# Performance work log

Hardware: AMD Instinct MI355X
Metric: run time of the kernel (lower is better)

The kernel has to match this reference:

```python
import jax, jax.numpy as jnp
import numpy as np

B, S, T = 32, 512, 128   # batch, source chars, target (protoform) chars
V, L = 128, 5            # char vocab len(C2I), number of languages
E, H, F = 512, 1024, 2048  # embedding_dim, model_size, feedforward_dim
START_CHAR, SEP_LANG = 1, L - 1


def setup_inputs() -> dict:
    key = jax.random.key(0)
    ks = jax.random.split(key, 32)
    f32 = jnp.float32

    def n(k, shape, fan_in):
        return jax.random.normal(k, shape, dtype=f32) * (1.0 / np.sqrt(fan_in))

    inp = {
        "src_chars": jax.random.randint(ks[0], (B, S), 0, V),
        "src_langs": jax.random.randint(ks[1], (B, S), 0, L),
        "tgt_chars": jax.random.randint(ks[2], (B, T), 0, V),
        # embedding feature extractor
        "char_emb": jax.random.normal(ks[3], (V, E), dtype=f32) * 0.02,
        "lang_emb": jax.random.normal(ks[4], (L, E), dtype=f32) * 0.02,
        "fc_W": n(ks[5], (E, 2 * E), 2 * E),
        "fc_b": jnp.zeros((E,), f32),
        # encoder GRU (PyTorch gate layout r,z,n)
        "enc_Wi": n(ks[6], (3 * H, E), E),
        "enc_Wh": n(ks[7], (3 * H, H), H),
        "enc_bi": jnp.zeros((3 * H,), f32),
        "enc_bh": jnp.zeros((3 * H,), f32),
        # decoder GRU, input = [E ; H]
        "dec_Wi": n(ks[8], (3 * H, E + H), E + H),
        "dec_Wh": n(ks[9], (3 * H, H), H),
        "dec_bi": jnp.zeros((3 * H,), f32),
        "dec_bh": jnp.zeros((3 * H,), f32),
        # attention
        "Wq": n(ks[10], (H, H), H),
        "Wk": n(ks[11], (H, H), H),
        "Wcs": n(ks[12], (H, E), E),
        # MLP H -> 2F -> F -> V
        "W1": n(ks[13], (2 * F, H), H),
        "b1": jnp.zeros((2 * F,), f32),
        "W2": n(ks[14], (F, 2 * F), 2 * F),
        "b2": jnp.zeros((F,), f32),
        "W3": n(ks[15], (V, F), F),
    }
    return inp


def _gru_step(h, x, Wi, Wh, bi, bh):
    gi = x @ Wi.T + bi            # [B, 3H]
    gh = h @ Wh.T + bh            # [B, 3H]
    ir, iz, inn = jnp.split(gi, 3, axis=-1)
    hr, hz, hn = jnp.split(gh, 3, axis=-1)
    r = jax.nn.sigmoid(ir + hr)
    z = jax.nn.sigmoid(iz + hz)
    n = jnp.tanh(inn + r * hn)
    return (1.0 - z) * n + z * h


def _mlp(x, W1, b1, W2, b2, W3):
    h = jax.nn.relu(x @ W1.T + b1)
    h = jax.nn.relu(h @ W2.T + b2)
    return h @ W3.T               # [B, V]


def reference(src_chars, src_langs, tgt_chars,
              char_emb, lang_emb, fc_W, fc_b,
              enc_Wi, enc_Wh, enc_bi, enc_bh,
              dec_Wi, dec_Wh, dec_bi, dec_bh,
              Wq, Wk, Wcs,
              W1, b1, W2, b2, W3):
    # --- feature extraction: concat(char_emb, lang_emb) -> Linear(2E -> E) ---
    def embed(c_idx, l_idx):
        ce = char_emb[c_idx]                       # [..., E]
        le = lang_emb[l_idx]                       # [..., E]
        return jnp.concatenate([ce, le], -1) @ fc_W.T + fc_b

    encoded = embed(src_chars, src_langs)          # [B, S, E]

    # --- encoder GRU over source chars ---
    def enc_step(h, x_t):
        h = _gru_step(h, x_t, enc_Wi, enc_Wh, enc_bi, enc_bh)
        return h, h

    h0 = jnp.zeros((encoded.shape[0], enc_Wh.shape[1]), encoded.dtype)
    _, enc_states = jax.lax.scan(enc_step, h0, jnp.swapaxes(encoded, 0, 1))
    enc_states = jnp.swapaxes(enc_states, 0, 1)    # [B, S, H]

    # precompute attention values: W_c_s(encoded) + W_key(keys)  [B, S, H]
    att_vals = encoded @ Wcs.T + enc_states @ Wk.T

    # --- initial decoder step: <s> embedding + last encoder state ---
    start_emb = embed(jnp.full((encoded.shape[0],), START_CHAR),
                      jnp.full((encoded.shape[0],), SEP_LANG))  # [B, E]
    context0 = enc_states[:, -1]                   # [B, H]
    d0 = jnp.zeros_like(context0)
    dec_h = _gru_step(d0, jnp.concatenate([start_emb, context0], -1),
                      dec_Wi, dec_Wh, dec_bi, dec_bh)

    tgt_emb = embed(tgt_chars, jnp.full_like(tgt_chars, SEP_LANG))  # [B, T, E]

    # --- decode T steps with teacher forcing ---
    def dec_step(carry, x_t):
        h, ctx = carry
        scores_t = _mlp(h + ctx, W1, b1, W2, b2, W3)           # [B, V]
        q = h @ Wq.T                                           # [B, H]
        att = jnp.einsum('bsh,bh->bs', enc_states, q)
        w = jax.nn.softmax(att, axis=-1)
        ctx_new = jnp.einsum('bs,bsh->bh', w, att_vals)        # [B, H]
        h_new = _gru_step(h, jnp.concatenate([x_t, ctx_new], -1),
                          dec_Wi, dec_Wh, dec_bi, dec_bh)
        return (h_new, ctx_new), scores_t

    (_, _), scores = jax.lax.scan(dec_step, (dec_h, context0),
                                  jnp.swapaxes(tgt_emb, 0, 1))
    return jnp.swapaxes(scores, 0, 1)              # [B, T, V]
```

## Files before the change

kernel.cpp:

```cpp
#include <hip/hip_runtime.h>
#include <math.h>


#define Bb 32
#define Ss 512
#define Tt 128
#define Vv 128
#define Hh 1024
#define H3 3072
#define APAD 40
#define NBE 64

typedef __attribute__((ext_vector_type(8))) short bf16x8;
typedef __attribute__((ext_vector_type(4))) float f32x4;

__device__ inline f32x4 mfma_bf16(bf16x8 a, bf16x8 b, f32x4 c) {
  return __builtin_amdgcn_mfma_f32_16x16x32_bf16(a, b, c, 0, 0, 0);
}
__device__ inline unsigned short f2bf(float f) {
  unsigned u = __builtin_bit_cast(unsigned, f);
  unsigned r = (u + 0x7fffu + ((u >> 16) & 1u)) >> 16;
  return (unsigned short)r;
}
__device__ inline float lof(unsigned u) { return __builtin_bit_cast(float, u << 16); }
__device__ inline float hif(unsigned u) { return __builtin_bit_cast(float, u & 0xffff0000u); }
__device__ inline float bf2f(unsigned short h) {
  return __builtin_bit_cast(float, ((unsigned)h) << 16);
}

#define O_ESBF   0UL
#define O_ESQ    33554432UL
#define O_AVBF   67108864UL
#define O_HCBF   100663296UL
#define O_WHE    109051904UL
#define O_WHD    115343360UL
#define O_WIC    121634816UL
#define O_WKB    127926272UL
#define O_WQT    130023424UL
#define O_W1B    132120576UL
#define O_W2B    140509184UL
#define O_W3B    157286400UL
#define O_XCAT   157810688UL
#define O_EMBFC  160432128UL
#define O_GITAB  161742848UL
#define O_AVTAB  169607168UL
#define O_DGIXT  172228608UL
#define O_GH     173801472UL
#define O_GI     174194688UL
#define O_H      174587904UL
#define O_HBF    174718976UL
#define O_CTX    174784512UL
#define O_CTXBF  174915584UL
#define O_ATTL   174981120UL

__global__ void k_xcat(const float* __restrict__ ce, const float* __restrict__ le,
                       float* __restrict__ xcat) {
  int row = blockIdx.x;
  int l = row >> 7, c = row & 127;
  int i = threadIdx.x * 4;
  float4 v;
  if (i < 512) v = *(const float4*)(ce + c * 512 + i);
  else         v = *(const float4*)(le + l * 512 + (i - 512));
  *(float4*)(xcat + (size_t)row * 1024 + i) = v;
}

__global__ void k_cltab(const int* __restrict__ sc, const int* __restrict__ sl,
                        int* __restrict__ cl, int* __restrict__ bar) {
  if (blockIdx.x == 0 && threadIdx.x == 0) *bar = 0;
  int i = blockIdx.x * 256 + threadIdx.x;
  int b = i >> 9, s = i & 511;
  cl[s * 32 + b] = sl[b * Ss + s] * 128 + sc[b * Ss + s];
}

__global__ void k_cvt(const float* __restrict__ src, int ld, int lc,
                      unsigned short* __restrict__ dst) {
  size_t i = ((size_t)blockIdx.x * 256 + threadIdx.x) * 8;
  size_t r = i >> lc;
  int c = (int)(i & ((1u << lc) - 1));
  const float* s = src + r * (size_t)ld + c;
  float4 v0 = *(const float4*)s;
  float4 v1 = *(const float4*)(s + 4);
  union { unsigned short us[8]; uint4 u; } o;
  o.us[0] = f2bf(v0.x); o.us[1] = f2bf(v0.y); o.us[2] = f2bf(v0.z); o.us[3] = f2bf(v0.w);
  o.us[4] = f2bf(v1.x); o.us[5] = f2bf(v1.y); o.us[6] = f2bf(v1.z); o.us[7] = f2bf(v1.w);
  *(uint4*)(dst + i) = o.u;
}

__global__ void k_transcvt(const float* __restrict__ in, unsigned short* __restrict__ out) {
  __shared__ float t[32][33];
  int c0 = blockIdx.x * 32, r0 = blockIdx.y * 32;
  int tx = threadIdx.x, ty = threadIdx.y;
  for (int i = ty; i < 32; i += 8)
    t[i][tx] = in[(size_t)(r0 + i) * 1024 + c0 + tx];
  __syncthreads();
  for (int i = ty; i < 32; i += 8)
    out[(size_t)(c0 + i) * 1024 + r0 + tx] = f2bf(t[tx][i]);
}

template <bool BIAS>
__global__ __launch_bounds__(256) void k_gemm(
    const float* __restrict__ A, int lda, const float* __restrict__ W, int ldw,
    const float* __restrict__ bias, float* __restrict__ C, int ldc, int K) {
  __shared__ float As[8][128];
  __shared__ float Ws[8][128];
  int tid = threadIdx.x;
  int n0 = blockIdx.x * 128, m0 = blockIdx.y * 128;
  int tx = tid & 15, ty = tid >> 4;
  int lrow = tid >> 1, lseg = (tid & 1) * 4;
  const float* Ap = A + (size_t)(m0 + lrow) * lda + lseg;
  const float* Wp = W + (size_t)(n0 + lrow) * ldw + lseg;
  float acc[8][8];
#pragma unroll
  for (int i = 0; i < 8; ++i)
#pragma unroll
    for (int j = 0; j < 8; ++j) acc[i][j] = 0.f;
  for (int kt = 0; kt < K; kt += 8) {
    float4 av = *(const float4*)(Ap + kt);
    float4 wv = *(const float4*)(Wp + kt);
    __syncthreads();
    As[lseg + 0][lrow] = av.x; As[lseg + 1][lrow] = av.y;
    As[lseg + 2][lrow] = av.z; As[lseg + 3][lrow] = av.w;
    Ws[lseg + 0][lrow] = wv.x; Ws[lseg + 1][lrow] = wv.y;
    Ws[lseg + 2][lrow] = wv.z; Ws[lseg + 3][lrow] = wv.w;
    __syncthreads();
#pragma unroll
    for (int kk = 0; kk < 8; ++kk) {
      float a[8], b[8];
      *(float4*)(a + 0) = *(const float4*)(&As[kk][ty * 8 + 0]);
      *(float4*)(a + 4) = *(const float4*)(&As[kk][ty * 8 + 4]);
      *(float4*)(b + 0) = *(const float4*)(&Ws[kk][tx * 8 + 0]);
      *(float4*)(b + 4) = *(const float4*)(&Ws[kk][tx * 8 + 4]);
#pragma unroll
      for (int i = 0; i < 8; ++i)
#pragma unroll
        for (int j = 0; j < 8; ++j) acc[i][j] = fmaf(a[i], b[j], acc[i][j]);
    }
  }
#pragma unroll
  for (int i = 0; i < 8; ++i) {
    int r = m0 + ty * 8 + i;
#pragma unroll
    for (int j = 0; j < 8; ++j) {
      int c = n0 + tx * 8 + j;
      float v = acc[i][j];
      if (BIAS) v += bias[c];
      C[(size_t)r * ldc + c] = v;
    }
  }
}

template <int EPI, bool RELU, bool BIAS>
__global__ __launch_bounds__(256) void k_bgemm(
    const unsigned short* __restrict__ A, int lda,
    const unsigned short* __restrict__ W, int ldw,
    const float* __restrict__ bias, void* __restrict__ Cout, int ldc, int K,
    const float* __restrict__ avtab, const int* __restrict__ gl,
    const int* __restrict__ gc) {
  __shared__ unsigned short As[128 * APAD];
  __shared__ unsigned short Bs[128 * APAD];
  int tid = threadIdx.x;
  int n0 = blockIdx.x * 128, m0 = blockIdx.y * 128;
  int w = tid >> 6, l = tid & 63;
  int mw = (w & 1) * 64, nw = (w >> 1) * 64;
  int lrow = tid >> 1, lk = (tid & 1) * 16;
  const unsigned short* Ap = A + (size_t)(m0 + lrow) * lda + lk;
  const unsigned short* Wp = W + (size_t)(n0 + lrow) * ldw + lk;
  int fr = l & 15, fk = (l >> 4) * 8;
  f32x4 acc[4][4];
#pragma unroll
  for (int i = 0; i < 4; ++i)
#pragma unroll
    for (int j = 0; j < 4; ++j) acc[i][j] = (f32x4){0.f, 0.f, 0.f, 0.f};
  for (int kt = 0; kt < K; kt += 32) {
    uint4 a0 = *(const uint4*)(Ap + kt);
    uint4 a1 = *(const uint4*)(Ap + kt + 8);
    uint4 b0 = *(const uint4*)(Wp + kt);
    uint4 b1 = *(const uint4*)(Wp + kt + 8);
    __syncthreads();
    *(uint4*)&As[lrow * APAD + lk] = a0;
    *(uint4*)&As[lrow * APAD + lk + 8] = a1;
    *(uint4*)&Bs[lrow * APAD + lk] = b0;
    *(uint4*)&Bs[lrow * APAD + lk + 8] = b1;
    __syncthreads();
    bf16x8 af[4], bfg[4];
#pragma unroll
    for (int i = 0; i < 4; ++i) af[i] = *(const bf16x8*)&As[(mw + i * 16 + fr) * APAD + fk];
#pragma unroll
    for (int j = 0; j < 4; ++j) bfg[j] = *(const bf16x8*)&Bs[(nw + j * 16 + fr) * APAD + fk];
#pragma unroll
    for (int i = 0; i < 4; ++i)
#pragma unroll
      for (int j = 0; j < 4; ++j) acc[i][j] = mfma_bf16(af[i], bfg[j], acc[i][j]);
  }
#pragma unroll
  for (int i = 0; i < 4; ++i)
#pragma unroll
    for (int j = 0; j < 4; ++j) {
      int col = n0 + nw + j * 16 + fr;
#pragma unroll
      for (int r = 0; r < 4; ++r) {
        int row = m0 + mw + i * 16 + (l >> 4) * 4 + r;
        float v = acc[i][j][r];
        if (BIAS) v += bias[col];
        if (RELU) v = fmaxf(v, 0.f);
        if (EPI == 0) {
          ((unsigned short*)Cout)[(size_t)row * ldc + col] = f2bf(v);
        } else if (EPI == 1) {
          int cl = gl[row] * 128 + gc[row];
          ((unsigned short*)Cout)[(size_t)row * ldc + col] =
              f2bf(v + avtab[(size_t)cl * 1024 + col]);
        } else {
          int tt = row >> 5, bb = row & 31;
          ((float*)Cout)[(size_t)bb * (Tt * Vv) + tt * Vv + col] = v;
        }
      }
    }
}

__global__ __launch_bounds__(512) void k_enc_pers(
    const unsigned short* __restrict__ Whe, const float* __restrict__ gitab,
    const int* __restrict__ cltab, const float* __restrict__ bh,
    float* __restrict__ h, unsigned short* __restrict__ hbf0,
    unsigned short* __restrict__ hbf1, unsigned short* __restrict__ esb,
    int* __restrict__ bar) {
  __shared__ unsigned short Ws[48 * 1024];
  __shared__ f32x4 red[8 * 6 * 64];
  int tid = threadIdx.x;
  int blk = blockIdx.x;
  int w = tid >> 6, l = tid & 63;
  int fr = l & 15, q = l >> 4;
  int j = blk * 16 + fr;
  {
    uint4* dst = (uint4*)Ws;
    const uint4* src = (const uint4*)Whe;
#pragma unroll
    for (int it = 0; it < 12; ++it) {
      int idx = it * 512 + tid;
      int lr = idx >> 7, c = idx & 127;
      int grow = (lr >> 4) * 1024 + blk * 16 + (lr & 15);
      dst[lr * 128 + (c ^ (lr & 7))] = src[(size_t)grow * 128 + c];
    }
  }
  float bhr = bh[j], bhz = bh[1024 + j], bhn = bh[2048 + j];
  float hold[4] = {0.f, 0.f, 0.f, 0.f};
  __syncthreads();
  const bf16x8* Wsv = (const bf16x8*)Ws;
  for (int s = 0; s < Ss; ++s) {
    unsigned short* wb = (s & 1) ? hbf1 : hbf0;
    const unsigned short* rb = (s & 1) ? hbf0 : hbf1;
    float gi0[4], gi1[4], gi2[4];
    if (w < 2) {
#pragma unroll
      for (int r = 0; r < 4; ++r) {
        int b = w * 16 + q * 4 + r;
        int c = cltab[s * 32 + b];
        const float* gp = gitab + (size_t)c * H3 + j;
        gi0[r] = gp[0]; gi1[r] = gp[1024]; gi2[r] = gp[2048];
      }
    }
    f32x4 acc[2][3];
#pragma unroll
    for (int m = 0; m < 2; ++m)
#pragma unroll
      for (int g = 0; g < 3; ++g) acc[m][g] = (f32x4){0.f, 0.f, 0.f, 0.f};
    if (s > 0) {
      int kb = w * 128 + q * 8;
      const unsigned short* A0 = rb + fr * 1024 + kb;
#pragma unroll
      for (int kt = 0; kt < 128; kt += 32) {
        bf16x8 a0 = *(const bf16x8*)(A0 + kt);
        bf16x8 a1 = *(const bf16x8*)(A0 + 16 * 1024 + kt);
        int c8 = (kb + kt) >> 3;
#pragma unroll
        for (int g = 0; g < 3; ++g) {
          bf16x8 bw = Wsv[(g * 16 + fr) * 128 + (c8 ^ (fr & 7))];
          acc[0][g] = mfma_bf16(a0, bw, acc[0][g]);
          acc[1][g] = mfma_bf16(a1, bw, acc[1][g]);
        }
      }
    }
#pragma unroll
    for (int m = 0; m < 2; ++m)
#pragma unroll
      for (int g = 0; g < 3; ++g)
        red[(w * 6 + m * 3 + g) * 64 + l] = acc[m][g];
    __syncthreads();
    if (w < 2) {
      int m = w;
      f32x4 as_[3];
#pragma unroll
      for (int g = 0; g < 3; ++g) as_[g] = (f32x4){0.f, 0.f, 0.f, 0.f};
#pragma unroll
      for (int ww = 0; ww < 8; ++ww)
#pragma unroll
        for (int g = 0; g < 3; ++g)
          as_[g] = as_[g] + red[(ww * 6 + m * 3 + g) * 64 + l];
#pragma unroll
      for (int r = 0; r < 4; ++r) {
        int b = m * 16 + q * 4 + r;
        float ghr = bhr, ghz = bhz, ghn = bhn;
        ghr += as_[0][r]; ghz += as_[1][r]; ghn += as_[2][r];
        float rg = 1.f / (1.f + expf(-(gi0[r] + ghr)));
        float zg = 1.f / (1.f + expf(-(gi1[r] + ghz)));
        float ng = tanhf(gi2[r] + rg * ghn);
        float hn = (1.f - zg) * ng + zg * hold[r];
        hold[r] = hn;
        unsigned short hb = f2bf(hn);
        wb[b * 1024 + j] = hb;
        esb[((size_t)b * Ss + s) * 1024 + j] = hb;
        if (s == Ss - 1) h[b * 1024 + j] = hn;
      }
    }
    __syncthreads();
    if (tid == 0) {
      __hip_atomic_fetch_add(bar, 1, __ATOMIC_RELEASE, __HIP_MEMORY_SCOPE_AGENT);
      int tgt = NBE * (s + 1);
      while (__hip_atomic_load(bar, __ATOMIC_RELAXED, __HIP_MEMORY_SCOPE_AGENT) < tgt)
        __builtin_amdgcn_s_sleep(1);
      __builtin_amdgcn_fence(__ATOMIC_ACQUIRE, "agent");
    }
    __syncthreads();
  }
}

template <int MODE>
__global__ __launch_bounds__(512) void k_step(
    const unsigned short* __restrict__ Wh,
    const unsigned short* __restrict__ Abf,
    const float* __restrict__ gtab,
    const int* __restrict__ idx,
    const float* __restrict__ ghb,
    const float* __restrict__ bh,
    float* __restrict__ h,
    unsigned short* __restrict__ hbfW,
    unsigned short* __restrict__ esb,
    int s, int flags) {
  __shared__ f32x4 red[8 * 6 * 64];
  int tid = threadIdx.x;
  int w = tid >> 6, l = tid & 63;
  int fr = l & 15, q = l >> 4;
  int j = blockIdx.x * 16 + fr;
  f32x4 acc[2][3];
#pragma unroll
  for (int m = 0; m < 2; ++m)
#pragma unroll
    for (int g = 0; g < 3; ++g) acc[m][g] = (f32x4){0.f, 0.f, 0.f, 0.f};
  if (!(flags & 4)) {
    int kb = w * 128 + q * 8;
    const unsigned short* A0 = Abf + fr * 1024 + kb;
    const unsigned short* W0 = Wh + (size_t)j * 1024 + kb;
#pragma unroll
    for (int kt = 0; kt < 128; kt += 32) {
      bf16x8 a0 = *(const bf16x8*)(A0 + kt);
      bf16x8 a1 = *(const bf16x8*)(A0 + 16 * 1024 + kt);
      bf16x8 b0 = *(const bf16x8*)(W0 + kt);
      bf16x8 b1 = *(const bf16x8*)(W0 + 1024 * 1024 + kt);
      bf16x8 b2 = *(const bf16x8*)(W0 + 2048 * 1024 + kt);
      acc[0][0] = mfma_bf16(a0, b0, acc[0][0]);
      acc[1][0] = mfma_bf16(a1, b0, acc[1][0]);
      acc[0][1] = mfma_bf16(a0, b1, acc[0][1]);
      acc[1][1] = mfma_bf16(a1, b1, acc[1][1]);
      acc[0][2] = mfma_bf16(a0, b2, acc[0][2]);
      acc[1][2] = mfma_bf16(a1, b2, acc[1][2]);
    }
  }
#pragma unroll
  for (int m = 0; m < 2; ++m)
#pragma unroll
    for (int g = 0; g < 3; ++g)
      red[(w * 6 + m * 3 + g) * 64 + l] = acc[m][g];
  __syncthreads();
  if (w >= 2) return;
  int m = w;
  f32x4 as_[3];
#pragma unroll
  for (int g = 0; g < 3; ++g) as_[g] = (f32x4){0.f, 0.f, 0.f, 0.f};
#pragma unroll
  for (int ww = 0; ww < 8; ++ww)
#pragma unroll
    for (int g = 0; g < 3; ++g)
      as_[g] = as_[g] + red[(ww * 6 + m * 3 + g) * 64 + l];
  float bhr = bh[j], bhz = bh[1024 + j], bhn = bh[2048 + j];
#pragma unroll
  for (int r = 0; r < 4; ++r) {
    int b = m * 16 + q * 4 + r;
    int c = (MODE == 0) ? idx[s * 32 + b] : ((flags & 2) ? 1 : idx[b * Tt + s]);
    const float* gp = gtab + (size_t)c * H3 + j;
    float gir = gp[0], giz = gp[1024], gin = gp[2048];
    float ghr = bhr, ghz = bhz, ghn = bhn;
    if (MODE == 0) {
      ghr += as_[0][r]; ghz += as_[1][r]; ghn += as_[2][r];
    } else {
      gir += as_[0][r]; giz += as_[1][r]; gin += as_[2][r];
      if (!(flags & 1)) {
        const float* g2 = ghb + b * H3 + j;
        ghr += g2[0]; ghz += g2[1024]; ghn += g2[2048];
      }
    }
    float rg = 1.f / (1.f + expf(-(gir + ghr)));
    float zg = 1.f / (1.f + expf(-(giz + ghz)));
    float ng = tanhf(gin + rg * ghn);
    float hold = (flags & 1) ? 0.f : h[b * 1024 + j];
    float hn = (1.f - zg) * ng + zg * hold;
    h[b * 1024 + j] = hn;
    unsigned short hb = f2bf(hn);
    hbfW[b * 1024 + j] = hb;
    if (MODE == 0) esb[((size_t)b * Ss + s) * 1024 + j] = hb;
  }
}

__global__ __launch_bounds__(256) void k_rec(
    const unsigned short* __restrict__ A, const unsigned short* __restrict__ W,
    float* __restrict__ C, int N, int nrec,
    const unsigned short* __restrict__ esq, const float* __restrict__ h,
    const float* __restrict__ ctx, float* __restrict__ attL,
    unsigned short* __restrict__ hc) {
  __shared__ unsigned short As[32 * 1024];
  int tid = threadIdx.x;
  int id = blockIdx.x;
  if (id < nrec) {
    {
      const uint4* src = (const uint4*)A;
      uint4* dst = (uint4*)As;
#pragma unroll
      for (int i = 0; i < 16; ++i) {
        int c = i * 256 + tid;
        int m = c >> 7, kc = c & 127;
        dst[m * 128 + (kc ^ (m & 7))] = src[c];
      }
    }
    __syncthreads();
    int w = tid >> 6, l = tid & 63;
    int nb = id * 64 + w * 16;
    int fr = l & 15, fk8 = (l >> 4);
    const unsigned short* Wp = W + (size_t)(nb + fr) * 1024 + fk8 * 8;
    const bf16x8* Asv = (const bf16x8*)As;
    f32x4 acc0 = (f32x4){0.f, 0.f, 0.f, 0.f}, acc1 = acc0;
#pragma unroll 8
    for (int kt = 0; kt < 1024; kt += 32) {
      int kc8 = (kt >> 3) + fk8;
      bf16x8 bw = *(const bf16x8*)(Wp + kt);
      bf16x8 a0 = Asv[fr * 128 + (kc8 ^ (fr & 7))];
      bf16x8 a1 = Asv[(fr + 16) * 128 + (kc8 ^ (fr & 7))];
      acc0 = mfma_bf16(a0, bw, acc0);
      acc1 = mfma_bf16(a1, bw, acc1);
    }
    int col = nb + fr;
    int rb = (l >> 4) * 4;
#pragma unroll
    for (int r = 0; r < 4; ++r) {
      C[(size_t)(rb + r) * N + col] = acc0[r];
      C[(size_t)(rb + r + 16) * N + col] = acc1[r];
    }
  } else {
    float* hs = (float*)As;
    int a = id - nrec, b = a >> 3, sc = a & 7;
    for (int i = tid; i < 1024; i += 256) hs[i] = h[b * 1024 + i];
    __syncthreads();
    if (sc < 4) {
      int j = sc * 256 + tid;
      hc[b * 1024 + j] = f2bf(hs[j] + ctx[b * 1024 + j]);
    }
    int sg = tid >> 2, li = tid & 3;
    int s = sc * 64 + sg;
    const unsigned short* ep = esq + (size_t)(b * 512 + s) * 1024;
    float acc = 0.f;
#pragma unroll 4
    for (int i = 0; i < 32; ++i) {
      int k = (i * 4 + li) * 8;
      uint4 e = *(const uint4*)(ep + k);
      float4 h0 = *(const float4*)&hs[k];
      float4 h1 = *(const float4*)&hs[k + 4];
      acc += lof(e.x) * h0.x + hif(e.x) * h0.y + lof(e.y) * h0.z + hif(e.y) * h0.w +
             lof(e.z) * h1.x + hif(e.z) * h1.y + lof(e.w) * h1.z + hif(e.w) * h1.w;
    }
    acc += __shfl_xor(acc, 1);
    acc += __shfl_xor(acc, 2);
    if (li == 0) attL[b * 512 + s] = acc;
  }
}

__global__ void k_ctxinit(const float* __restrict__ h, float* __restrict__ ctx,
                          unsigned short* __restrict__ ctxbf) {
  int idx = blockIdx.x * 256 + threadIdx.x;
  float v = h[idx];
  ctx[idx] = v;
  ctxbf[idx] = f2bf(v);
}

__global__ __launch_bounds__(256) void k_ctxsm(const float* __restrict__ attL,
                                               const unsigned short* __restrict__ av,
                                               float* __restrict__ ctx,
                                               unsigned short* __restrict__ ctxbf) {
  int jt = blockIdx.x, b = blockIdx.y;
  __shared__ float w[512];
  __shared__ float wm[4];
  __shared__ float wsm[4];
  __shared__ float red2[128];
  int tid = threadIdx.x;
  float a0 = attL[b * Ss + tid * 2];
  float a1 = attL[b * Ss + tid * 2 + 1];
  float m = fmaxf(a0, a1);
  for (int d = 1; d < 64; d <<= 1) m = fmaxf(m, __shfl_xor(m, d));
  if ((tid & 63) == 0) wm[tid >> 6] = m;
  __syncthreads();
  m = fmaxf(fmaxf(wm[0], wm[1]), fmaxf(wm[2], wm[3]));
  float e0 = expf(a0 - m), e1 = expf(a1 - m);
  w[tid * 2] = e0;
  w[tid * 2 + 1] = e1;
  float ssum = e0 + e1;
  for (int d = 1; d < 64; d <<= 1) ssum += __shfl_xor(ssum, d);
  if ((tid & 63) == 0) wsm[tid >> 6] = ssum;
  __syncthreads();
  float scale = 1.f / (wsm[0] + wsm[1] + wsm[2] + wsm[3]);
  int j = jt * 128 + (tid & 127);
  int sh = tid >> 7;
  const unsigned short* avp = av + (size_t)(b * Ss + sh * 256) * Hh + j;
  float acc = 0.f;
#pragma unroll 16
  for (int s = 0; s < 256; ++s) acc += w[sh * 256 + s] * bf2f(avp[(size_t)s * Hh]);
  if (sh == 1) red2[tid & 127] = acc;
  __syncthreads();
  if (sh == 0) {
    float v = (acc + red2[tid & 127]) * scale;
    ctx[b * Hh + j] = v;
    ctxbf[b * Hh + j] = f2bf(v);
  }
}

extern "C" void kernel_launch(void* const* d_in, const int* in_sizes, int n_in,
                              void* d_out, int out_size, void* d_ws, size_t ws_size,
                              hipStream_t stream) {
  (void)in_sizes; (void)n_in; (void)out_size; (void)ws_size;
  const int*   src_chars = (const int*)d_in[0];
  const int*   src_langs = (const int*)d_in[1];
  const int*   tgt_chars = (const int*)d_in[2];
  const float* char_emb  = (const float*)d_in[3];
  const float* lang_emb  = (const float*)d_in[4];
  const float* fc_W  = (const float*)d_in[5];
  const float* fc_b  = (const float*)d_in[6];
  const float* enc_Wi = (const float*)d_in[7];
  const float* enc_Wh = (const float*)d_in[8];
  const float* enc_bi = (const float*)d_in[9];
  const float* enc_bh = (const float*)d_in[10];
  const float* dec_Wi = (const float*)d_in[11];
  const float* dec_Wh = (const float*)d_in[12];
  const float* dec_bi = (const float*)d_in[13];
  const float* dec_bh = (const float*)d_in[14];
  const float* Wq  = (const float*)d_in[15];
  const float* Wk  = (const float*)d_in[16];
  const float* Wcs = (const float*)d_in[17];
  const float* W1 = (const float*)d_in[18];
  const float* b1 = (const float*)d_in[19];
  const float* W2 = (const float*)d_in[20];
  const float* b2 = (const float*)d_in[21];
  const float* W3 = (const float*)d_in[22];
  float* out = (float*)d_out;

  char* ws = (char*)d_ws;
  unsigned short* esbf  = (unsigned short*)(ws + O_ESBF);
  unsigned short* esq   = (unsigned short*)(ws + O_ESQ);
  unsigned short* avbf  = (unsigned short*)(ws + O_AVBF);
  unsigned short* hcbf  = (unsigned short*)(ws + O_HCBF);
  unsigned short* WheB  = (unsigned short*)(ws + O_WHE);
  unsigned short* WhdB  = (unsigned short*)(ws + O_WHD);
  unsigned short* WicB  = (unsigned short*)(ws + O_WIC);
  unsigned short* WkB   = (unsigned short*)(ws + O_WKB);
  unsigned short* WqTB  = (unsigned short*)(ws + O_WQT);
  unsigned short* W1B   = (unsigned short*)(ws + O_W1B);
  unsigned short* W2B   = (unsigned short*)(ws + O_W2B);
  unsigned short* W3B   = (unsigned short*)(ws + O_W3B);
  float* xcat   = (float*)(ws + O_XCAT);
  float* embfc  = (float*)(ws + O_EMBFC);
  float* gitab  = (float*)(ws + O_GITAB);
  float* avtab  = (float*)(ws + O_AVTAB);
  float* dgixt  = (float*)(ws + O_DGIXT);
  float* ghbuf  = (float*)(ws + O_GH);
  float* h      = (float*)(ws + O_H);
  unsigned short* hbf   = (unsigned short*)(ws + O_HBF);
  float* ctx    = (float*)(ws + O_CTX);
  unsigned short* ctxbf = (unsigned short*)(ws + O_CTXBF);
  float* attL   = (float*)(ws + O_ATTL);
  unsigned short* G1 = esq;
  unsigned short* G2 = avbf;
  int* cltab = (int*)(ws + O_GI);
  unsigned short* hbf2 = (unsigned short*)(ws + O_GI + 65536);
  int* bar = (int*)(ws + O_GI + 131072);

  dim3 blk(256);

  k_xcat<<<640, blk, 0, stream>>>(char_emb, lang_emb, xcat);
  k_cltab<<<64, blk, 0, stream>>>(src_chars, src_langs, cltab, bar);
  k_gemm<true><<<dim3(4, 5), blk, 0, stream>>>(xcat, 1024, fc_W, 1024, fc_b, embfc, 512, 1024);
  k_gemm<true><<<dim3(24, 5), blk, 0, stream>>>(embfc, 512, enc_Wi, 512, enc_bi, gitab, H3, 512);
  k_gemm<false><<<dim3(8, 5), blk, 0, stream>>>(embfc, 512, Wcs, 512, nullptr, avtab, Hh, 512);
  k_gemm<true><<<dim3(24, 1), blk, 0, stream>>>(embfc + 512 * 512, 512, dec_Wi, 1536, dec_bi,
                                                dgixt, H3, 512);
  k_cvt<<<1536, blk, 0, stream>>>(enc_Wh, 1024, 10, WheB);
  k_cvt<<<1536, blk, 0, stream>>>(dec_Wh, 1024, 10, WhdB);
  k_cvt<<<1536, blk, 0, stream>>>(dec_Wi + 512, 1536, 10, WicB);
  k_cvt<<<512,  blk, 0, stream>>>(Wk, 1024, 10, WkB);
  k_cvt<<<2048, blk, 0, stream>>>(W1, 1024, 10, W1B);
  k_cvt<<<4096, blk, 0, stream>>>(W2, 4096, 12, W2B);
  k_cvt<<<128,  blk, 0, stream>>>(W3, 2048, 11, W3B);
  k_transcvt<<<dim3(32, 32), dim3(32, 8), 0, stream>>>(Wq, WqTB);

  {
    const unsigned short* p_whe = WheB;
    const float* p_git = gitab;
    const int* p_cl = cltab;
    const float* p_bh = enc_bh;
    float* p_h = h;
    unsigned short* p_h0 = hbf;
    unsigned short* p_h1 = hbf2;
    unsigned short* p_esb = esbf;
    int* p_bar = bar;
    void* kargs[] = {(void*)&p_whe, (void*)&p_git, (void*)&p_cl, (void*)&p_bh,
                     (void*)&p_h, (void*)&p_h0, (void*)&p_h1, (void*)&p_esb,
                     (void*)&p_bar};
    hipLaunchCooperativeKernel((const void*)k_enc_pers, dim3(NBE), dim3(512), kargs, 0, stream);
  }

  k_bgemm<0, false, false><<<dim3(8, 128), blk, 0, stream>>>(
      esbf, 1024, WqTB, 1024, nullptr, esq, 1024, 1024, nullptr, nullptr, nullptr);
  k_bgemm<1, false, false><<<dim3(8, 128), blk, 0, stream>>>(
      esbf, 1024, WkB, 1024, nullptr, avbf, 1024, 1024, avtab, src_langs, src_chars);

  k_ctxinit<<<128, blk, 0, stream>>>(h, ctx, ctxbf);
  k_step<1><<<64, 512, 0, stream>>>(WicB, ctxbf, dgixt, tgt_chars, nullptr, dec_bh,
                                    h, hbf, nullptr, 0, 3);

  for (int t = 0; t < Tt; ++t) {
    k_rec<<<304, blk, 0, stream>>>(hbf, WhdB, ghbuf, H3, 48,
                                   esq, h, ctx, attL, hcbf + (size_t)t * Bb * Hh);
    if (t == Tt - 1) break;
    k_ctxsm<<<dim3(8, 32), blk, 0, stream>>>(attL, avbf, ctx, ctxbf);
    k_step<1><<<64, 512, 0, stream>>>(WicB, ctxbf, dgixt, tgt_chars, ghbuf, dec_bh,
                                      h, hbf, nullptr, t, 0);
  }

  k_bgemm<0, true, true><<<dim3(32, 32), blk, 0, stream>>>(
      hcbf, 1024, W1B, 1024, b1, G1, 4096, 1024, nullptr, nullptr, nullptr);
  k_bgemm<0, true, true><<<dim3(16, 32), blk, 0, stream>>>(
      G1, 4096, W2B, 4096, b2, G2, 2048, 4096, nullptr, nullptr, nullptr);
  k_bgemm<2, false, false><<<dim3(1, 32), blk, 0, stream>>>(
      G2, 2048, W3B, 2048, nullptr, out, 0, 2048, nullptr, nullptr, nullptr);
}
```

Baseline: 8.790 ms.

## Fuse decoder time loop into one persistent cooperative kernel with grid barriers

Replaces the per-timestep launches of k_rec, k_ctxsm and k_step with a single cooperative persistent kernel of 256 blocks. Inside it, blocks take roles: half the first 128 hold the decoder Wh slice and the other half the context Wi slice, both kept in LDS, while the remaining blocks compute attention logits and the softmax-weighted context. Steps are separated by a global atomic barrier. The goal is to remove hundreds of kernel launch gaps and repeated weight reloads from global memory, at the cost of three grid barriers per step and fewer, bigger-LDS blocks doing the work.

New measurement: 13.42 ms. 52.7% more time.

```diff
diff --git a/kernel.cpp b/kernel.cpp
--- a/kernel.cpp
+++ b/kernel.cpp
@@ -10,6 +10,7 @@
 #define H3 3072
 #define APAD 40
 #define NBE 64
+#define NBD 256
 
 typedef __attribute__((ext_vector_type(8))) short bf16x8;
 typedef __attribute__((ext_vector_type(4))) float f32x4;
@@ -26,6 +27,19 @@
 __device__ inline float hif(unsigned u) { return __builtin_bit_cast(float, u & 0xffff0000u); }
 __device__ inline float bf2f(unsigned short h) {
   return __builtin_bit_cast(float, ((unsigned)h) << 16);
+}
+
+__device__ inline void gbar(int* bar, int nb, int& bc) {
+  __syncthreads();
+  if (threadIdx.x == 0) {
+    __hip_atomic_fetch_add(bar, 1, __ATOMIC_RELEASE, __HIP_MEMORY_SCOPE_AGENT);
+    ++bc;
+    int tgt = nb * bc;
+    while (__hip_atomic_load(bar, __ATOMIC_RELAXED, __HIP_MEMORY_SCOPE_AGENT) < tgt)
+      __builtin_amdgcn_s_sleep(1);
+    __builtin_amdgcn_fence(__ATOMIC_ACQUIRE, "agent");
+  }
+  __syncthreads();
 }
 
 #define O_ESBF   0UL
@@ -66,7 +80,7 @@
 
 __global__ void k_cltab(const int* __restrict__ sc, const int* __restrict__ sl,
                         int* __restrict__ cl, int* __restrict__ bar) {
-  if (blockIdx.x == 0 && threadIdx.x == 0) *bar = 0;
+  if (blockIdx.x == 0 && threadIdx.x == 0) { bar[0] = 0; bar[32] = 0; }
   int i = blockIdx.x * 256 + threadIdx.x;
   int b = i >> 9, s = i & 511;
   cl[s * 32 + b] = sl[b * Ss + s] * 128 + sc[b * Ss + s];
@@ -245,6 +259,7 @@
   float hold[4] = {0.f, 0.f, 0.f, 0.f};
   __syncthreads();
   const bf16x8* Wsv = (const bf16x8*)Ws;
+  int bc = 0;
   for (int s = 0; s < Ss; ++s) {
     unsigned short* wb = (s & 1) ? hbf1 : hbf0;
     const unsigned short* rb = (s & 1) ? hbf0 : hbf1;
@@ -298,8 +313,7 @@
 #pragma unroll
       for (int r = 0; r < 4; ++r) {
         int b = m * 16 + q * 4 + r;
-        float ghr = bhr, ghz = bhz, ghn = bhn;
-        ghr += as_[0][r]; ghz += as_[1][r]; ghn += as_[2][r];
+        float ghr = bhr + as_[0][r], ghz = bhz + as_[1][r], ghn = bhn + as_[2][r];
         float rg = 1.f / (1.f + expf(-(gi0[r] + ghr)));
         float zg = 1.f / (1.f + expf(-(gi1[r] + ghz)));
         float ng = tanhf(gi2[r] + rg * ghn);
@@ -311,220 +325,276 @@
         if (s == Ss - 1) h[b * 1024 + j] = hn;
       }
     }
-    __syncthreads();
-    if (tid == 0) {
-      __hip_atomic_fetch_add(bar, 1, __ATOMIC_RELEASE, __HIP_MEMORY_SCOPE_AGENT);
-      int tgt = NBE * (s + 1);
-      while (__hip_atomic_load(bar, __ATOMIC_RELAXED, __HIP_MEMORY_SCOPE_AGENT) < tgt)
-        __builtin_amdgcn_s_sleep(1);
-      __builtin_amdgcn_fence(__ATOMIC_ACQUIRE, "agent");
-    }
-    __syncthreads();
-  }
-}
-
-template <int MODE>
-__global__ __launch_bounds__(512) void k_step(
-    const unsigned short* __restrict__ Wh,
-    const unsigned short* __restrict__ Abf,
-    const float* __restrict__ gtab,
-    const int* __restrict__ idx,
-    const float* __restrict__ ghb,
-    const float* __restrict__ bh,
-    float* __restrict__ h,
-    unsigned short* __restrict__ hbfW,
-    unsigned short* __restrict__ esb,
-    int s, int flags) {
-  __shared__ f32x4 red[8 * 6 * 64];
+    gbar(bar, NBE, bc);
+  }
+}
+
+__global__ __launch_bounds__(256) void k_dec_pers(
+    const unsigned short* __restrict__ Whd, const unsigned short* __restrict__ Wic,
+    const unsigned short* __restrict__ esq, const unsigned short* __restrict__ av,
+    const float* __restrict__ dgixt, const int* __restrict__ tgt,
+    const float* __restrict__ bh, float* __restrict__ h,
+    unsigned short* __restrict__ hbf, float* __restrict__ ctx,
+    unsigned short* __restrict__ ctxbf, float* __restrict__ attL,
+    float* __restrict__ ghbuf, unsigned short* __restrict__ hcbf,
+    int* __restrict__ bar) {
+  __shared__ unsigned short Ws[48 * 1024];
+  __shared__ f32x4 red[4 * 6 * 64];
+  __shared__ float hs[1024];
+  __shared__ float wS[512];
+  __shared__ float wm[4], wsm[4];
+  __shared__ float red2[128];
   int tid = threadIdx.x;
-  int w = tid >> 6, l = tid & 63;
+  int blk = blockIdx.x;
+  int wv = tid >> 6, l = tid & 63;
   int fr = l & 15, q = l >> 4;
-  int j = blockIdx.x * 16 + fr;
-  f32x4 acc[2][3];
-#pragma unroll
-  for (int m = 0; m < 2; ++m)
-#pragma unroll
-    for (int g = 0; g < 3; ++g) acc[m][g] = (f32x4){0.f, 0.f, 0.f, 0.f};
-  if (!(flags & 4)) {
-    int kb = w * 128 + q * 8;
-    const unsigned short* A0 = Abf + fr * 1024 + kb;
-    const unsigned short* W0 = Wh + (size_t)j * 1024 + kb;
-#pragma unroll
-    for (int kt = 0; kt < 128; kt += 32) {
+  int bc = 0;
+  int jsl = (blk & 63) * 16;
+  if (blk < 128) {
+    const uint4* src = (const uint4*)((blk < 64) ? Whd : Wic);
+    uint4* dst = (uint4*)Ws;
+#pragma unroll
+    for (int it = 0; it < 24; ++it) {
+      int idx = it * 256 + tid;
+      int lr = idx >> 7, c = idx & 127;
+      int grow = (lr >> 4) * 1024 + jsl + (lr & 15);
+      dst[lr * 128 + (c ^ (lr & 7))] = src[(size_t)grow * 128 + c];
+    }
+  }
+  const bf16x8* Wsv = (const bf16x8*)Ws;
+  int jw = jsl + fr;
+  float bhr = bh[jw], bhz = bh[1024 + jw], bhn = bh[2048 + jw];
+  if (blk < 128) {
+    int idx = blk * 256 + tid;
+    float v = h[idx];
+    ctx[idx] = v;
+    ctxbf[idx] = f2bf(v);
+  }
+  gbar(bar, NBD, bc);
+  if (blk >= 64 && blk < 128) {
+    f32x4 acc[2][3];
+#pragma unroll
+    for (int m = 0; m < 2; ++m)
+#pragma unroll
+      for (int g = 0; g < 3; ++g) acc[m][g] = (f32x4){0.f, 0.f, 0.f, 0.f};
+    int kb = wv * 256 + q * 8;
+    const unsigned short* A0 = ctxbf + fr * 1024 + kb;
+#pragma unroll
+    for (int kt = 0; kt < 256; kt += 32) {
       bf16x8 a0 = *(const bf16x8*)(A0 + kt);
       bf16x8 a1 = *(const bf16x8*)(A0 + 16 * 1024 + kt);
-      bf16x8 b0 = *(const bf16x8*)(W0 + kt);
-      bf16x8 b1 = *(const bf16x8*)(W0 + 1024 * 1024 + kt);
-      bf16x8 b2 = *(const bf16x8*)(W0 + 2048 * 1024 + kt);
-      acc[0][0] = mfma_bf16(a0, b0, acc[0][0]);
-      acc[1][0] = mfma_bf16(a1, b0, acc[1][0]);
-      acc[0][1] = mfma_bf16(a0, b1, acc[0][1]);
-      acc[1][1] = mfma_bf16(a1, b1, acc[1][1]);
-      acc[0][2] = mfma_bf16(a0, b2, acc[0][2]);
-      acc[1][2] = mfma_bf16(a1, b2, acc[1][2]);
-    }
-  }
-#pragma unroll
-  for (int m = 0; m < 2; ++m)
-#pragma unroll
-    for (int g = 0; g < 3; ++g)
-      red[(w * 6 + m * 3 + g) * 64 + l] = acc[m][g];
-  __syncthreads();
-  if (w >= 2) return;
-  int m = w;
-  f32x4 as_[3];
-#pragma unroll
-  for (int g = 0; g < 3; ++g) as_[g] = (f32x4){0.f, 0.f, 0.f, 0.f};
-#pragma unroll
-  for (int ww = 0; ww < 8; ++ww)
-#pragma unroll
-    for (int g = 0; g < 3; ++g)
-      as_[g] = as_[g] + red[(ww * 6 + m * 3 + g) * 64 + l];
-  float bhr = bh[j], bhz = bh[1024 + j], bhn = bh[2048 + j];
-#pragma unroll
-  for (int r = 0; r < 4; ++r) {
-    int b = m * 16 + q * 4 + r;
-    int c = (MODE == 0) ? idx[s * 32 + b] : ((flags & 2) ? 1 : idx[b * Tt + s]);
-    const float* gp = gtab + (size_t)c * H3 + j;
-    float gir = gp[0], giz = gp[1024], gin = gp[2048];
-    float ghr = bhr, ghz = bhz, ghn = bhn;
-    if (MODE == 0) {
-      ghr += as_[0][r]; ghz += as_[1][r]; ghn += as_[2][r];
-    } else {
-      gir += as_[0][r]; giz += as_[1][r]; gin += as_[2][r];
-      if (!(flags & 1)) {
-        const float* g2 = ghb + b * H3 + j;
-        ghr += g2[0]; ghz += g2[1024]; ghn += g2[2048];
-      }
-    }
-    float rg = 1.f / (1.f + expf(-(gir + ghr)));
-    float zg = 1.f / (1.f + expf(-(giz + ghz)));
-    float ng = tanhf(gin + rg * ghn);
-    float hold = (flags & 1) ? 0.f : h[b * 1024 + j];
-    float hn = (1.f - zg) * ng + zg * hold;
-    h[b * 1024 + j] = hn;
-    unsigned short hb = f2bf(hn);
-    hbfW[b * 1024 + j] = hb;
-    if (MODE == 0) esb[((size_t)b * Ss + s) * 1024 + j] = hb;
-  }
-}
-
-__global__ __launch_bounds__(256) void k_rec(
-    const unsigned short* __restrict__ A, const unsigned short* __restrict__ W,
-    float* __restrict__ C, int N, int nrec,
-    const unsigned short* __restrict__ esq, const float* __restrict__ h,
-    const float* __restrict__ ctx, float* __restrict__ attL,
-    unsigned short* __restrict__ hc) {
-  __shared__ unsigned short As[32 * 1024];
-  int tid = threadIdx.x;
-  int id = blockIdx.x;
-  if (id < nrec) {
+      int c8 = (kb + kt) >> 3;
+#pragma unroll
+      for (int g = 0; g < 3; ++g) {
+        bf16x8 bw = Wsv[(g * 16 + fr) * 128 + (c8 ^ (fr & 7))];
+        acc[0][g] = mfma_bf16(a0, bw, acc[0][g]);
+        acc[1][g] = mfma_bf16(a1, bw, acc[1][g]);
+      }
+    }
+#pragma unroll
+    for (int m = 0; m < 2; ++m)
+#pragma unroll
+      for (int g = 0; g < 3; ++g)
+        red[(wv * 6 + m * 3 + g) * 64 + l] = acc[m][g];
+    __syncthreads();
+    if (wv < 2) {
+      int m = wv;
+      f32x4 as_[3];
+#pragma unroll
+      for (int g = 0; g < 3; ++g) as_[g] = (f32x4){0.f, 0.f, 0.f, 0.f};
+#pragma unroll
+      for (int ww = 0; ww < 4; ++ww)
+#pragma unroll
+        for (int g = 0; g < 3; ++g)
+          as_[g] = as_[g] + red[(ww * 6 + m * 3 + g) * 64 + l];
+#pragma unroll
+      for (int r = 0; r < 4; ++r) {
+        int b = m * 16 + q * 4 + r;
+        const float* gp = dgixt + (size_t)1 * H3 + jw;
+        float gir = gp[0] + as_[0][r];
+        float giz = gp[1024] + as_[1][r];
+        float gin = gp[2048] + as_[2][r];
+        float rg = 1.f / (1.f + expf(-(gir + bhr)));
+        float zg = 1.f / (1.f + expf(-(giz + bhz)));
+        float ng = tanhf(gin + rg * bhn);
+        float hn = (1.f - zg) * ng;
+        h[b * 1024 + jw] = hn;
+        hbf[b * 1024 + jw] = f2bf(hn);
+      }
+    }
+  }
+  gbar(bar, NBD, bc);
+  for (int t = 0; t < Tt; ++t) {
+    if (blk >= 128) {
+      int ab = (blk - 128) >> 2, aq = (blk - 128) & 3;
+      for (int i = tid; i < 1024; i += 256) hs[i] = h[ab * 1024 + i];
+      __syncthreads();
+      {
+        int j2 = aq * 256 + tid;
+        hcbf[(size_t)t * (Bb * Hh) + ab * 1024 + j2] = f2bf(hs[j2] + ctx[ab * 1024 + j2]);
+      }
+      int sg = tid >> 2, li = tid & 3;
+      int s0 = aq * 128 + sg;
+      const unsigned short* ep0 = esq + (size_t)(ab * 512 + s0) * 1024;
+      const unsigned short* ep1 = ep0 + 64 * 1024;
+      float acc0 = 0.f, acc1 = 0.f;
+#pragma unroll 4
+      for (int i = 0; i < 32; ++i) {
+        int k = (i * 4 + li) * 8;
+        uint4 e0 = *(const uint4*)(ep0 + k);
+        uint4 e1 = *(const uint4*)(ep1 + k);
+        float4 h0 = *(const float4*)&hs[k];
+        float4 h1 = *(const float4*)&hs[k + 4];
+        acc0 += lof(e0.x) * h0.x + hif(e0.x) * h0.y + lof(e0.y) * h0.z + hif(e0.y) * h0.w +
+                lof(e0.z) * h1.x + hif(e0.z) * h1.y + lof(e0.w) * h1.z + hif(e0.w) * h1.w;
+        acc1 += lof(e1.x) * h0.x + hif(e1.x) * h0.y + lof(e1.y) * h0.z + hif(e1.y) * h0.w +
+                lof(e1.z) * h1.x + hif(e1.z) * h1.y + lof(e1.w) * h1.z + hif(e1.w) * h1.w;
+      }
+      acc0 += __shfl_xor(acc0, 1);
+      acc0 += __shfl_xor(acc0, 2);
+      acc1 += __shfl_xor(acc1, 1);
+      acc1 += __shfl_xor(acc1, 2);
+      if (li == 0) {
+        attL[ab * 512 + s0] = acc0;
+        attL[ab * 512 + s0 + 64] = acc1;
+      }
+    } else if (blk < 64) {
+      f32x4 acc[2][3];
+#pragma unroll
+      for (int m = 0; m < 2; ++m)
+#pragma unroll
+        for (int g = 0; g < 3; ++g) acc[m][g] = (f32x4){0.f, 0.f, 0.f, 0.f};
+      int kb = wv * 256 + q * 8;
+      const unsigned short* A0 = hbf + fr * 1024 + kb;
+#pragma unroll
+      for (int kt = 0; kt < 256; kt += 32) {
+        bf16x8 a0 = *(const bf16x8*)(A0 + kt);
+        bf16x8 a1 = *(const bf16x8*)(A0 + 16 * 1024 + kt);
+        int c8 = (kb + kt) >> 3;
+#pragma unroll
+        for (int g = 0; g < 3; ++g) {
+          bf16x8 bw = Wsv[(g * 16 + fr) * 128 + (c8 ^ (fr & 7))];
+          acc[0][g] = mfma_bf16(a0, bw, acc[0][g]);
+          acc[1][g] = mfma_bf16(a1, bw, acc[1][g]);
+        }
+      }
+#pragma unroll
+      for (int m = 0; m < 2; ++m)
+#pragma unroll
+        for (int g = 0; g < 3; ++g)
+          red[(wv * 6 + m * 3 + g) * 64 + l] = acc[m][g];
+      __syncthreads();
+      if (wv < 2) {
+        int m = wv;
+        f32x4 as_[3];
+#pragma unroll
+        for (int g = 0; g < 3; ++g) as_[g] = (f32x4){0.f, 0.f, 0.f, 0.f};
+#pragma unroll
+        for (int ww = 0; ww < 4; ++ww)
+#pragma unroll
+          for (int g = 0; g < 3; ++g)
+            as_[g] = as_[g] + red[(ww * 6 + m * 3 + g) * 64 + l];
+#pragma unroll
+        for (int r = 0; r < 4; ++r) {
+          int b = m * 16 + q * 4 + r;
+#pragma unroll
+          for (int g = 0; g < 3; ++g)
+            ghbuf[b * H3 + g * 1024 + jw] = as_[g][r];
+        }
+      }
+    }
+    if (t == Tt - 1) break;
+    gbar(bar, NBD, bc);
     {
-      const uint4* src = (const uint4*)A;
-      uint4* dst = (uint4*)As;
-#pragma unroll
-      for (int i = 0; i < 16; ++i) {
-        int c = i * 256 + tid;
-        int m = c >> 7, kc = c & 127;
-        dst[m * 128 + (kc ^ (m & 7))] = src[c];
-      }
-    }
-    __syncthreads();
-    int w = tid >> 6, l = tid & 63;
-    int nb = id * 64 + w * 16;
-    int fr = l & 15, fk8 = (l >> 4);
-    const unsigned short* Wp = W + (size_t)(nb + fr) * 1024 + fk8 * 8;
-    const bf16x8* Asv = (const bf16x8*)As;
-    f32x4 acc0 = (f32x4){0.f, 0.f, 0.f, 0.f}, acc1 = acc0;
-#pragma unroll 8
-    for (int kt = 0; kt < 1024; kt += 32) {
-      int kc8 = (kt >> 3) + fk8;
-      bf16x8 bw = *(const bf16x8*)(Wp + kt);
-      bf16x8 a0 = Asv[fr * 128 + (kc8 ^ (fr & 7))];
-      bf16x8 a1 = Asv[(fr + 16) * 128 + (kc8 ^ (fr & 7))];
-      acc0 = mfma_bf16(a0, bw, acc0);
-      acc1 = mfma_bf16(a1, bw, acc1);
-    }
-    int col = nb + fr;
-    int rb = (l >> 4) * 4;
-#pragma unroll
-    for (int r = 0; r < 4; ++r) {
-      C[(size_t)(rb + r) * N + col] = acc0[r];
-      C[(size_t)(rb + r + 16) * N + col] = acc1[r];
-    }
-  } else {
-    float* hs = (float*)As;
-    int a = id - nrec, b = a >> 3, sc = a & 7;
-    for (int i = tid; i < 1024; i += 256) hs[i] = h[b * 1024 + i];
-    __syncthreads();
-    if (sc < 4) {
-      int j = sc * 256 + tid;
-      hc[b * 1024 + j] = f2bf(hs[j] + ctx[b * 1024 + j]);
-    }
-    int sg = tid >> 2, li = tid & 3;
-    int s = sc * 64 + sg;
-    const unsigned short* ep = esq + (size_t)(b * 512 + s) * 1024;
-    float acc = 0.f;
-#pragma unroll 4
-    for (int i = 0; i < 32; ++i) {
-      int k = (i * 4 + li) * 8;
-      uint4 e = *(const uint4*)(ep + k);
-      float4 h0 = *(const float4*)&hs[k];
-      float4 h1 = *(const float4*)&hs[k + 4];
-      acc += lof(e.x) * h0.x + hif(e.x) * h0.y + lof(e.y) * h0.z + hif(e.y) * h0.w +
-             lof(e.z) * h1.x + hif(e.z) * h1.y + lof(e.w) * h1.z + hif(e.w) * h1.w;
-    }
-    acc += __shfl_xor(acc, 1);
-    acc += __shfl_xor(acc, 2);
-    if (li == 0) attL[b * 512 + s] = acc;
-  }
-}
-
-__global__ void k_ctxinit(const float* __restrict__ h, float* __restrict__ ctx,
-                          unsigned short* __restrict__ ctxbf) {
-  int idx = blockIdx.x * 256 + threadIdx.x;
-  float v = h[idx];
-  ctx[idx] = v;
-  ctxbf[idx] = f2bf(v);
-}
-
-__global__ __launch_bounds__(256) void k_ctxsm(const float* __restrict__ attL,
-                                               const unsigned short* __restrict__ av,
-                                               float* __restrict__ ctx,
-                                               unsigned short* __restrict__ ctxbf) {
-  int jt = blockIdx.x, b = blockIdx.y;
-  __shared__ float w[512];
-  __shared__ float wm[4];
-  __shared__ float wsm[4];
-  __shared__ float red2[128];
-  int tid = threadIdx.x;
-  float a0 = attL[b * Ss + tid * 2];
-  float a1 = attL[b * Ss + tid * 2 + 1];
-  float m = fmaxf(a0, a1);
-  for (int d = 1; d < 64; d <<= 1) m = fmaxf(m, __shfl_xor(m, d));
-  if ((tid & 63) == 0) wm[tid >> 6] = m;
-  __syncthreads();
-  m = fmaxf(fmaxf(wm[0], wm[1]), fmaxf(wm[2], wm[3]));
-  float e0 = expf(a0 - m), e1 = expf(a1 - m);
-  w[tid * 2] = e0;
-  w[tid * 2 + 1] = e1;
-  float ssum = e0 + e1;
-  for (int d = 1; d < 64; d <<= 1) ssum += __shfl_xor(ssum, d);
-  if ((tid & 63) == 0) wsm[tid >> 6] = ssum;
-  __syncthreads();
-  float scale = 1.f / (wsm[0] + wsm[1] + wsm[2] + wsm[3]);
-  int j = jt * 128 + (tid & 127);
-  int sh = tid >> 7;
-  const unsigned short* avp = av + (size_t)(b * Ss + sh * 256) * Hh + j;
-  float acc = 0.f;
+      int b2 = blk >> 3, jt = blk & 7;
+      float a0 = attL[b2 * Ss + tid * 2];
+      float a1 = attL[b2 * Ss + tid * 2 + 1];
+      float m = fmaxf(a0, a1);
+      for (int d = 1; d < 64; d <<= 1) m = fmaxf(m, __shfl_xor(m, d));
+      if ((tid & 63) == 0) wm[tid >> 6] = m;
+      __syncthreads();
+      m = fmaxf(fmaxf(wm[0], wm[1]), fmaxf(wm[2], wm[3]));
+      float e0 = expf(a0 - m), e1 = expf(a1 - m);
+      wS[tid * 2] = e0;
+      wS[tid * 2 + 1] = e1;
+      float ssum = e0 + e1;
+      for (int d = 1; d < 64; d <<= 1) ssum += __shfl_xor(ssum, d);
+      if ((tid & 63) == 0) wsm[tid >> 6] = ssum;
+      __syncthreads();
+      float scale = 1.f / (wsm[0] + wsm[1] + wsm[2] + wsm[3]);
+      int j = jt * 128 + (tid & 127);
+      int sh = tid >> 7;
+      const unsigned short* avp = av + (size_t)(b2 * Ss + sh * 256) * Hh + j;
+      float acc = 0.f;
 #pragma unroll 16
-  for (int s = 0; s < 256; ++s) acc += w[sh * 256 + s] * bf2f(avp[(size_t)s * Hh]);
-  if (sh == 1) red2[tid & 127] = acc;
-  __syncthreads();
-  if (sh == 0) {
-    float v = (acc + red2[tid & 127]) * scale;
-    ctx[b * Hh + j] = v;
-    ctxbf[b * Hh + j] = f2bf(v);
+      for (int s = 0; s < 256; ++s) acc += wS[sh * 256 + s] * bf2f(avp[(size_t)s * Hh]);
+      if (sh == 1) red2[tid & 127] = acc;
+      __syncthreads();
+      if (sh == 0) {
+        float v = (acc + red2[tid & 127]) * scale;
+        ctx[b2 * Hh + j] = v;
+        ctxbf[b2 * Hh + j] = f2bf(v);
+      }
+    }
+    gbar(bar, NBD, bc);
+    if (blk >= 64 && blk < 128) {
+      f32x4 acc[2][3];
+#pragma unroll
+      for (int m = 0; m < 2; ++m)
+#pragma unroll
+        for (int g = 0; g < 3; ++g) acc[m][g] = (f32x4){0.f, 0.f, 0.f, 0.f};
+      int kb = wv * 256 + q * 8;
+      const unsigned short* A0 = ctxbf + fr * 1024 + kb;
+#pragma unroll
+      for (int kt = 0; kt < 256; kt += 32) {
+        bf16x8 a0 = *(const bf16x8*)(A0 + kt);
+        bf16x8 a1 = *(const bf16x8*)(A0 + 16 * 1024 + kt);
+        int c8 = (kb + kt) >> 3;
+#pragma unroll
+        for (int g = 0; g < 3; ++g) {
+          bf16x8 bw = Wsv[(g * 16 + fr) * 128 + (c8 ^ (fr & 7))];
+          acc[0][g] = mfma_bf16(a0, bw, acc[0][g]);
+          acc[1][g] = mfma_bf16(a1, bw, acc[1][g]);
+        }
+      }
+#pragma unroll
+      for (int m = 0; m < 2; ++m)
+#pragma unroll
+        for (int g = 0; g < 3; ++g)
+          red[(wv * 6 + m * 3 + g) * 64 + l] = acc[m][g];
+      __syncthreads();
+      if (wv < 2) {
+        int m = wv;
+        f32x4 as_[3];
+#pragma unroll
+        for (int g = 0; g < 3; ++g) as_[g] = (f32x4){0.f, 0.f, 0.f, 0.f};
+#pragma unroll
+        for (int ww = 0; ww < 4; ++ww)
+#pragma unroll
+          for (int g = 0; g < 3; ++g)
+            as_[g] = as_[g] + red[(ww * 6 + m * 3 + g) * 64 + l];
+#pragma unroll
+        for (int r = 0; r < 4; ++r) {
+          int b = m * 16 + q * 4 + r;
+          int c = tgt[b * Tt + t];
+          const float* gp = dgixt + (size_t)c * H3 + jw;
+          float gir = gp[0] + as_[0][r];
+          float giz = gp[1024] + as_[1][r];
+          float gin = gp[2048] + as_[2][r];
+          const float* g2 = ghbuf + b * H3 + jw;
+          float ghr = bhr + g2[0];
+          float ghz = bhz + g2[1024];
+          float ghn = bhn + g2[2048];
+          float rg = 1.f / (1.f + expf(-(gir + ghr)));
+          float zg = 1.f / (1.f + expf(-(giz + ghz)));
+          float ng = tanhf(gin + rg * ghn);
+          float hn = (1.f - zg) * ng + zg * h[b * 1024 + jw];
+          h[b * 1024 + jw] = hn;
+          hbf[b * 1024 + jw] = f2bf(hn);
+        }
+      }
+    }
+    gbar(bar, NBD, bc);
   }
 }
 
@@ -626,17 +696,27 @@
   k_bgemm<1, false, false><<<dim3(8, 128), blk, 0, stream>>>(
       esbf, 1024, WkB, 1024, nullptr, avbf, 1024, 1024, avtab, src_langs, src_chars);
 
-  k_ctxinit<<<128, blk, 0, stream>>>(h, ctx, ctxbf);
-  k_step<1><<<64, 512, 0, stream>>>(WicB, ctxbf, dgixt, tgt_chars, nullptr, dec_bh,
-                                    h, hbf, nullptr, 0, 3);
-
-  for (int t = 0; t < Tt; ++t) {
-    k_rec<<<304, blk, 0, stream>>>(hbf, WhdB, ghbuf, H3, 48,
-                                   esq, h, ctx, attL, hcbf + (size_t)t * Bb * Hh);
-    if (t == Tt - 1) break;
-    k_ctxsm<<<dim3(8, 32), blk, 0, stream>>>(attL, avbf, ctx, ctxbf);
-    k_step<1><<<64, 512, 0, stream>>>(WicB, ctxbf, dgixt, tgt_chars, ghbuf, dec_bh,
-                                      h, hbf, nullptr, t, 0);
+  {
+    const unsigned short* p_whd = WhdB;
+    const unsigned short* p_wic = WicB;
+    const unsigned short* p_esq = esq;
+    const unsigned short* p_av = avbf;
+    const float* p_dgixt = dgixt;
+    const int* p_tgt = tgt_chars;
+    const float* p_bh = dec_bh;
+    float* p_h = h;
+    unsigned short* p_hbf = hbf;
+    float* p_ctx = ctx;
+    unsigned short* p_ctxbf = ctxbf;
+    float* p_attL = attL;
+    float* p_gh = ghbuf;
+    unsigned short* p_hc = hcbf;
+    int* p_bar = bar + 32;
+    void* kargs[] = {(void*)&p_whd, (void*)&p_wic, (void*)&p_esq, (void*)&p_av,
+                     (void*)&p_dgixt, (void*)&p_tgt, (void*)&p_bh, (void*)&p_h,
+                     (void*)&p_hbf, (void*)&p_ctx, (void*)&p_ctxbf, (void*)&p_attL,
+                     (void*)&p_gh, (void*)&p_hc, (void*)&p_bar};
+    hipLaunchCooperativeKernel((const void*)k_dec_pers, dim3(NBD), dim3(256), kargs, 0, stream);
   }
 
   k_bgemm<0, true, true><<<dim3(32, 32), blk, 0, stream>>>(
```
